# Performance work log

Hardware: AMD Instinct MI355X
Metric: run time of the kernel (lower is better)

The kernel has to match this reference:

```python
import jax, jax.numpy as jnp
import numpy as np

N = 100000   # nodes
E = 1600000  # edges
IN = 128     # in_node_channels
H = 128      # hidden_channels
EPS = 1e-5   # BatchNorm eps


def _gcn_conv(x, W, b, src, dst, n):
    # x' = W x, then symmetric-normalized aggregation with self-loops (PyG GCNConv)
    xw = x @ W                                             # [N, H]
    loop = jnp.arange(n, dtype=src.dtype)
    src_f = jnp.concatenate([src, loop])                   # [E+N]
    dst_f = jnp.concatenate([dst, loop])
    deg = jax.ops.segment_sum(jnp.ones(src_f.shape, xw.dtype), dst_f, num_segments=n)
    dis = jax.lax.rsqrt(jnp.maximum(deg, 1.0))             # deg >= 1 due to self-loops
    norm = dis[src_f] * dis[dst_f]                         # [E+N]
    msg = xw[src_f] * norm[:, None]                        # gather + scale
    out = jax.ops.segment_sum(msg, dst_f, num_segments=n)  # scatter-add
    return out + b


def _bn(x, gamma, beta):
    # training-mode BatchNorm1d over the node dimension
    m = jnp.mean(x, axis=0)
    v = jnp.mean(jnp.square(x - m), axis=0)
    return gamma * (x - m) * jax.lax.rsqrt(v + EPS) + beta


def setup_inputs() -> dict:
    key = jax.random.key(0)
    ks = jax.random.split(key, 8)
    glorot = lambda k, shape, fan: jax.random.normal(k, shape, jnp.float32) / np.sqrt(fan).astype(np.float32)
    x = jax.random.normal(ks[0], (N, IN), jnp.float32)
    edge_index = jax.random.randint(ks[1], (2, E), 0, N, dtype=jnp.int32)
    return {
        "x": x,
        "edge_index": edge_index,
        "W1": glorot(ks[2], (IN, H), IN), "b1": jnp.zeros((H,), jnp.float32),
        "g1": jnp.ones((H,), jnp.float32), "be1": jnp.zeros((H,), jnp.float32),
        "W2": glorot(ks[3], (H, H), H), "b2": jnp.zeros((H,), jnp.float32),
        "g2": jnp.ones((H,), jnp.float32), "be2": jnp.zeros((H,), jnp.float32),
        "Wm1": glorot(ks[4], (H, 64), H), "bm1": jnp.zeros((64,), jnp.float32),
        "Wm2": glorot(ks[5], (64, 1), 64), "bm2": jnp.zeros((1,), jnp.float32),
    }


def reference(x, edge_index, W1, b1, g1, be1, W2, b2, g2, be2, Wm1, bm1, Wm2, bm2):
    src, dst = edge_index[0], edge_index[1]
    h = jax.nn.relu(_bn(_gcn_conv(x, W1, b1, src, dst, N), g1, be1))
    h = jax.nn.relu(_bn(_gcn_conv(h, W2, b2, src, dst, N), g2, be2))
    # MLP head (dropout is identity in eval / deterministic reference)
    h = jax.nn.relu(h @ Wm1 + bm1)
    out = h @ Wm2 + bm2                                     # [N, 1]
    return jnp.squeeze(out, axis=-1)                        # [N]
```

## Files before the change

### kernel.cpp

```cpp
#include <hip/hip_runtime.h>
#include <hip/hip_fp16.h>

#define HC 128
#define EPS_BN 1e-5f
#define NSTRIPE 8
#define AGG_BLOCKS 3072
#define BSHIFT 9
#define BNODES (1 << BSHIFT)
#define BCAP 12288
#define CHUNK 8192
#define SRC_BITS 18

typedef _Float16 f16;
typedef f16  f16x8 __attribute__((ext_vector_type(8)));
typedef float f32x4 __attribute__((ext_vector_type(4)));

__global__ __launch_bounds__(1024) void edge_bin(const int* __restrict__ src,
                                                 const int* __restrict__ dst,
                                                 int* __restrict__ gcur,
                                                 unsigned int* __restrict__ packed, int E) {
    __shared__ int cnt[256];
    __shared__ int cur[256];
    const int tid = threadIdx.x;
    const int e0 = blockIdx.x * CHUNK;
    int dreg[8];
    if (tid < 256) cnt[tid] = 0;
    __syncthreads();
#pragma unroll
    for (int i = 0; i < 8; ++i) {
        int e = e0 + i * 1024 + tid;
        dreg[i] = (e < E) ? dst[e] : -1;
        if (dreg[i] >= 0) atomicAdd(&cnt[dreg[i] >> BSHIFT], 1);
    }
    __syncthreads();
    if (tid < 256) cur[tid] = (cnt[tid] > 0) ? atomicAdd(&gcur[tid], cnt[tid]) : 0;
    __syncthreads();
#pragma unroll
    for (int i = 0; i < 8; ++i) {
        int e = e0 + i * 1024 + tid;
        if (dreg[i] >= 0) {
            int s = src[e];
            int b = dreg[i] >> BSHIFT;
            int pos = b * BCAP + atomicAdd(&cur[b], 1);
            packed[pos] = ((unsigned)(dreg[i] & (BNODES - 1)) << SRC_BITS) | (unsigned)s;
        }
    }
}

__global__ __launch_bounds__(1024) void sort_wprep(const unsigned int* __restrict__ packed,
                                                   const int* __restrict__ gcur,
                                                   int2* __restrict__ rowptr2,
                                                   float* __restrict__ dis,
                                                   int* __restrict__ srcs, int n, int nbSort,
                                                   const float* __restrict__ W1,
                                                   const float* __restrict__ W2,
                                                   const float* __restrict__ Wm1,
                                                   f16* __restrict__ Wt1,
                                                   f16* __restrict__ Wt2,
                                                   f16* __restrict__ Wm1t) {
    if (blockIdx.x >= nbSort) {
        int idx = (blockIdx.x - nbSort) * 1024 + threadIdx.x;
        if (idx < 16384) {
            int k = idx >> 7, c = idx & 127;
            Wt1[(size_t)c * HC + k] = (f16)W1[idx];
        } else if (idx < 32768) {
            int i = idx - 16384;
            int k = i >> 7, c = i & 127;
            Wt2[(size_t)c * HC + k] = (f16)W2[i];
        } else if (idx < 40960) {
            int i = idx - 32768;
            int c = i >> 7, k = i & 127;
            Wm1t[(size_t)c * HC + k] = (f16)Wm1[(size_t)k * 64 + c];
        }
        return;
    }
    __shared__ int cnt[BNODES];
    __shared__ int cur[BNODES];
    __shared__ int scn[BNODES];
    const int b = blockIdx.x;
    const int node0 = b << BSHIFT;
    const int tid = threadIdx.x;
    const int base = b * BCAP;
    const int end  = base + gcur[b];

    if (tid < BNODES) cnt[tid] = 0;
    __syncthreads();
    for (int e = base + tid; e < end; e += 1024)
        atomicAdd(&cnt[packed[e] >> SRC_BITS], 1);
    __syncthreads();
    if (tid < BNODES) scn[tid] = cnt[tid];
    __syncthreads();
    for (int off = 1; off < BNODES; off <<= 1) {
        int t = 0;
        if (tid < BNODES && tid >= off) t = scn[tid - off];
        __syncthreads();
        if (tid < BNODES) scn[tid] += t;
        __syncthreads();
    }
    if (tid < BNODES) {
        int excl = scn[tid] - cnt[tid];
        int node = node0 + tid;
        if (node < n) {
            rowptr2[node] = make_int2(base + excl, base + excl + cnt[tid]);
            dis[node] = rsqrtf((float)cnt[tid] + 1.f);
        }
        cur[tid] = excl;
    }
    __syncthreads();
    for (int e = base + tid; e < end; e += 1024) {
        unsigned p = packed[e];
        int pos = atomicAdd(&cur[p >> SRC_BITS], 1);
        srcs[base + pos] = (int)(p & ((1u << SRC_BITS) - 1));
    }
}

template<int SRC_F16, int TRANS>
__global__ __launch_bounds__(512) void gemm_mfma(const void* __restrict__ Xv,
                                                 const f16* __restrict__ Wt,
                                                 const float* __restrict__ stats,
                                                 const float* __restrict__ gamma,
                                                 const float* __restrict__ beta,
                                                 const float* __restrict__ dis,
                                                 f16* __restrict__ Y, int n) {
    __shared__ f16 Ah[128][136];
    __shared__ f16 Bh[128][136];
    __shared__ float sc[HC], sh[HC];
    const int tid  = threadIdx.x;
    const int row0 = blockIdx.x * 128;

    if constexpr (TRANS) {
        if (tid < 128) {
            float s = 0.f, q = 0.f;
#pragma unroll
            for (int t = 0; t < NSTRIPE; ++t) {
                s += stats[t * 256 + tid];
                q += stats[t * 256 + 128 + tid];
            }
            float m = s / (float)n;
            float v = q / (float)n - m * m;
            float scv = gamma[tid] * rsqrtf(fmaxf(v, 0.f) + EPS_BN);
            sc[tid] = scv;
            sh[tid] = beta[tid] - m * scv;
        }
    }

#pragma unroll
    for (int i = 0; i < 4; ++i) {
        int idx = i * 512 + tid;
        int r = idx >> 4, g = idx & 15;
        *(f16x8*)&Bh[r][g * 8] = *(const f16x8*)(Wt + (size_t)r * HC + g * 8);
    }
    __syncthreads();

#pragma unroll
    for (int i = 0; i < 4; ++i) {
        int idx = i * 512 + tid;
        int r = idx >> 4, g = idx & 15;
        int grow = row0 + r;
        f16x8 h = {};
        if (grow < n) {
            if constexpr (SRC_F16) {
                f16x8 v = *(const f16x8*)((const f16*)Xv + (size_t)grow * HC + g * 8);
                if constexpr (TRANS) {
#pragma unroll
                    for (int j = 0; j < 8; ++j) {
                        float f = (float)v[j];
                        f = fmaxf(fmaf(f, sc[g * 8 + j], sh[g * 8 + j]), 0.f);
                        h[j] = (f16)f;
                    }
                } else h = v;
            } else {
                const float* X = (const float*)Xv;
                float4 a = *(const float4*)(X + (size_t)grow * HC + g * 8);
                float4 c = *(const float4*)(X + (size_t)grow * HC + g * 8 + 4);
                h[0] = (f16)a.x; h[1] = (f16)a.y; h[2] = (f16)a.z; h[3] = (f16)a.w;
                h[4] = (f16)c.x; h[5] = (f16)c.y; h[6] = (f16)c.z; h[7] = (f16)c.w;
            }
        }
        *(f16x8*)&Ah[r][g * 8] = h;
    }
    __syncthreads();

    const int wv   = tid >> 6;
    const int lane = tid & 63;
    const int m    = lane & 15;
    const int kq   = (lane >> 4) * 8;

    f32x4 acc[8] = {};
#pragma unroll
    for (int kc = 0; kc < HC; kc += 32) {
        f16x8 a = *(const f16x8*)&Ah[wv * 16 + m][kc + kq];
#pragma unroll
        for (int t = 0; t < 8; ++t) {
            f16x8 b = *(const f16x8*)&Bh[t * 16 + m][kc + kq];
            acc[t] = __builtin_amdgcn_mfma_f32_16x16x32_f16(a, b, acc[t], 0, 0, 0);
        }
    }

    __syncthreads();
    {
        const int rg = (lane >> 4) * 4;
        float dv[4];
#pragma unroll
        for (int r = 0; r < 4; ++r) {
            int grow = row0 + wv * 16 + rg + r;
            dv[r] = (grow < n) ? dis[grow] : 0.f;
        }
#pragma unroll
        for (int t = 0; t < 8; ++t)
#pragma unroll
            for (int r = 0; r < 4; ++r)
                Ah[wv * 16 + rg + r][t * 16 + m] = (f16)(acc[t][r] * dv[r]);
    }
    __syncthreads();
#pragma unroll
    for (int i = 0; i < 4; ++i) {
        int idx = i * 512 + tid;
        int r = idx >> 4, g = idx & 15;
        int grow = row0 + r;
        if (grow < n)
            *(f16x8*)(Y + (size_t)grow * HC + g * 8) = *(const f16x8*)&Ah[r][g * 8];
    }
}

__global__ __launch_bounds__(256) void gcn_agg_f16(const f16* __restrict__ xws,
                                                   const int* __restrict__ srcs,
                                                   const int2* __restrict__ rowptr2,
                                                   const float* __restrict__ dis,
                                                   const float* __restrict__ bias,
                                                   f16* __restrict__ out,
                                                   float* __restrict__ stats,
                                                   int n, int nwaves) {
    __shared__ float lds_s[4][128], lds_q[4][128];
    const int wv   = threadIdx.x >> 6;
    const int lane = threadIdx.x & 63;
    const int g    = lane >> 4;
    const int cg   = lane & 15;

    float b8[8];
#pragma unroll
    for (int j = 0; j < 8; ++j) b8[j] = bias[cg * 8 + j];

    float s8[8] = {}, q8[8] = {};

    for (int node = blockIdx.x * 4 + wv; node < n; node += nwaves) {
        const int2 rp = rowptr2[node];
        const int e1 = rp.y;
        float acc[8] = {};
        int e  = rp.x;
        int i0 = e + g, i1 = i0 + 4;
        int s0 = (i0 < e1) ? srcs[i0] : n;
        int s1 = (i1 < e1) ? srcs[i1] : n;
        while (e < e1) {
            int en = e + 8;
            int j0 = en + g, j1 = j0 + 4;
            int t0 = (j0 < e1) ? srcs[j0] : n;
            int t1 = (j1 < e1) ? srcs[j1] : n;
            f16x8 v0 = *(const f16x8*)(xws + (size_t)s0 * HC + cg * 8);
            f16x8 v1 = *(const f16x8*)(xws + (size_t)s1 * HC + cg * 8);
            f16x8 p = v0 + v1;
#pragma unroll
            for (int j = 0; j < 8; ++j)
                acc[j] += (float)p[j];
            s0 = t0; s1 = t1; e = en;
        }
#pragma unroll
        for (int j = 0; j < 8; ++j) acc[j] += __shfl_xor(acc[j], 16);
#pragma unroll
        for (int j = 0; j < 8; ++j) acc[j] += __shfl_xor(acc[j], 32);

        if (g == 0) {
            float dv = dis[node];
            f16x8 self = *(const f16x8*)(xws + (size_t)node * HC + cg * 8);
            f16x8 o;
#pragma unroll
            for (int j = 0; j < 8; ++j) {
                float r = fmaf(acc[j] + (float)self[j], dv, b8[j]);
                o[j] = (f16)r;
                s8[j] += r;
                q8[j] += r * r;
            }
            *(f16x8*)(out + (size_t)node * HC + cg * 8) = o;
        }
    }

    if (g == 0) {
#pragma unroll
        for (int j = 0; j < 8; ++j) {
            lds_s[wv][cg * 8 + j] = s8[j];
            lds_q[wv][cg * 8 + j] = q8[j];
        }
    }
    __syncthreads();
    float* stripe = stats + (size_t)(blockIdx.x & (NSTRIPE - 1)) * 256;
    if (threadIdx.x < 128) {
        float s = lds_s[0][threadIdx.x] + lds_s[1][threadIdx.x] +
                  lds_s[2][threadIdx.x] + lds_s[3][threadIdx.x];
        float q = lds_q[0][threadIdx.x] + lds_q[1][threadIdx.x] +
                  lds_q[2][threadIdx.x] + lds_q[3][threadIdx.x];
        atomicAdd(&stripe[threadIdx.x], s);
        atomicAdd(&stripe[128 + threadIdx.x], q);
    }
}

__global__ __launch_bounds__(256) void mlp_mfma(const f16* __restrict__ h,
                                                const float* __restrict__ stats,
                                                const float* __restrict__ gamma,
                                                const float* __restrict__ beta,
                                                const f16* __restrict__ Wm1t,
                                                const float* __restrict__ bm1,
                                                const float* __restrict__ Wm2,
                                                const float* __restrict__ bm2,
                                                float* __restrict__ out, int n) {
    __shared__ f16 Hs[64][136];
    __shared__ f16 Ws[64][136];
    __shared__ float sc[HC], sh[HC], bmv[64], w2v[64];
    const int tid  = threadIdx.x;
    const int row0 = blockIdx.x * 64;

    if (tid < 128) {
        float s = 0.f, q = 0.f;
#pragma unroll
        for (int t = 0; t < NSTRIPE; ++t) {
            s += stats[t * 256 + tid];
            q += stats[t * 256 + 128 + tid];
        }
        float m = s / (float)n;
        float v = q / (float)n - m * m;
        float scv = gamma[tid] * rsqrtf(fmaxf(v, 0.f) + EPS_BN);
        sc[tid] = scv;
        sh[tid] = beta[tid] - m * scv;
    }
    if (tid < 64) { bmv[tid] = bm1[tid]; w2v[tid] = Wm2[tid]; }

#pragma unroll
    for (int i = 0; i < 4; ++i) {
        int idx = i * 256 + tid;
        int r = idx >> 4, g = idx & 15;
        *(f16x8*)&Ws[r][g * 8] = *(const f16x8*)(Wm1t + (size_t)r * HC + g * 8);
    }
    __syncthreads();

#pragma unroll
    for (int i = 0; i < 4; ++i) {
        int idx = i * 256 + tid;
        int r = idx >> 4, g = idx & 15;
        int grow = row0 + r;
        f16x8 hv = {};
        if (grow < n) {
            f16x8 v = *(const f16x8*)(h + (size_t)grow * HC + g * 8);
#pragma unroll
            for (int j = 0; j < 8; ++j) {
                float f = (float)v[j];
                f = fmaxf(fmaf(f, sc[g * 8 + j], sh[g * 8 + j]), 0.f);
                hv[j] = (f16)f;
            }
        }
        *(f16x8*)&Hs[r][g * 8] = hv;
    }
    __syncthreads();

    const int wv   = tid >> 6;
    const int lane = tid & 63;
    const int m    = lane & 15;
    const int kq   = (lane >> 4) * 8;

    f32x4 acc[4] = {};
#pragma unroll
    for (int kc = 0; kc < HC; kc += 32) {
        f16x8 a = *(const f16x8*)&Hs[wv * 16 + m][kc + kq];
#pragma unroll
        for (int t = 0; t < 4; ++t) {
            f16x8 b = *(const f16x8*)&Ws[t * 16 + m][kc + kq];
            acc[t] = __builtin_amdgcn_mfma_f32_16x16x32_f16(a, b, acc[t], 0, 0, 0);
        }
    }

    float part[4];
#pragma unroll
    for (int reg = 0; reg < 4; ++reg) {
        float s = 0.f;
#pragma unroll
        for (int t = 0; t < 4; ++t) {
            int col = t * 16 + m;
            s += fmaxf(acc[t][reg] + bmv[col], 0.f) * w2v[col];
        }
        part[reg] = s;
    }
#pragma unroll
    for (int off = 1; off < 16; off <<= 1) {
#pragma unroll
        for (int reg = 0; reg < 4; ++reg)
            part[reg] += __shfl_xor(part[reg], off);
    }
    if (m == 0) {
        int rbase = row0 + wv * 16 + (lane >> 4) * 4;
        float bb = bm2[0];
#pragma unroll
        for (int reg = 0; reg < 4; ++reg) {
            int row = rbase + reg;
            if (row < n) out[row] = part[reg] + bb;
        }
    }
}

extern "C" void kernel_launch(void* const* d_in, const int* in_sizes, int n_in,
                              void* d_out, int out_size, void* d_ws, size_t ws_size,
                              hipStream_t stream) {
    const float* x   = (const float*)d_in[0];
    const int*   ei  = (const int*)  d_in[1];
    const float* W1  = (const float*)d_in[2];
    const float* b1  = (const float*)d_in[3];
    const float* g1  = (const float*)d_in[4];
    const float* be1 = (const float*)d_in[5];
    const float* W2  = (const float*)d_in[6];
    const float* b2  = (const float*)d_in[7];
    const float* g2  = (const float*)d_in[8];
    const float* be2 = (const float*)d_in[9];
    const float* Wm1 = (const float*)d_in[10];
    const float* bm1 = (const float*)d_in[11];
    const float* Wm2 = (const float*)d_in[12];
    const float* bm2 = (const float*)d_in[13];
    float* out = (float*)d_out;

    const int n = in_sizes[0] / HC;
    const int E = in_sizes[1] / 2;
    const int* srcp = ei;
    const int* dstp = ei + E;
    const int nb = (n + BNODES - 1) >> BSHIFT;

    char* ws = (char*)d_ws;
    size_t off = 0;
    auto alloc = [&](size_t bytes) { void* p = ws + off; off = (off + bytes + 511) & ~511ULL; return p; };
    float*  dis     = (float*) alloc((size_t)n * 4);
    int2*   rowptr2 = (int2*)  alloc((size_t)n * 8);
    int*    gcur    = (int*)   alloc(1024);
    float*  stats   = (float*) alloc(2 * NSTRIPE * 256 * 4);
    float*  stats1  = stats;
    float*  stats2  = stats + NSTRIPE * 256;
    unsigned int* packed = (unsigned int*)alloc((size_t)nb * BCAP * 4);
    int*    srcs    = (int*)   alloc((size_t)nb * BCAP * 4);
    f16*    xws     = (f16*)   alloc((size_t)(n + 1) * HC * 2);
    f16*    bufBh   = (f16*)   alloc((size_t)n * HC * 2);
    f16*    Wt1     = (f16*)   alloc((size_t)HC * HC * 2);
    f16*    Wt2     = (f16*)   alloc((size_t)HC * HC * 2);
    f16*    Wm1t    = (f16*)   alloc((size_t)64 * HC * 2);

    const int gemmBlocks = (n + 127) / 128;
    const int mlpBlocks  = (n + 63) / 64;
    const int binBlocks  = (E + CHUNK - 1) / CHUNK;
    const int wprepBlks  = 40;
    const int aggWaves   = AGG_BLOCKS * 4;

    hipMemsetAsync(gcur, 0, 1024 + 2 * NSTRIPE * 256 * 4, stream);
    hipMemsetAsync(xws + (size_t)n * HC, 0, HC * 2, stream);

    edge_bin<<<binBlocks, 1024, 0, stream>>>(srcp, dstp, gcur, packed, E);
    sort_wprep<<<nb + wprepBlks, 1024, 0, stream>>>(packed, gcur, rowptr2, dis, srcs, n, nb,
                                                    W1, W2, Wm1, Wt1, Wt2, Wm1t);

    gemm_mfma<0, 0><<<gemmBlocks, 512, 0, stream>>>(x, Wt1, nullptr, nullptr, nullptr,
                                                    dis, xws, n);
    gcn_agg_f16<<<AGG_BLOCKS, 256, 0, stream>>>(xws, srcs, rowptr2, dis, b1,
                                                bufBh, stats1, n, aggWaves);

    gemm_mfma<1, 1><<<gemmBlocks, 512, 0, stream>>>(bufBh, Wt2, stats1, g1, be1,
                                                    dis, xws, n);
    gcn_agg_f16<<<AGG_BLOCKS, 256, 0, stream>>>(xws, srcs, rowptr2, dis, b2,
                                                bufBh, stats2, n, aggWaves);

    mlp_mfma<<<mlpBlocks, 256, 0, stream>>>(bufBh, stats2, g2, be2, Wm1t, bm1, Wm2, bm2,
                                            out, n);
}
```

Baseline: 313.9 us.

## Fuse edge binning with first GEMM and move degree scaling into sort

The edge-binning pass, the first-layer GEMM (now reading fp32 W1 directly and transposing it into shared memory) and the weight prep for W2/Wm1 are merged into one launch, so the GEMM no longer waits on degree computation. The dis scaling of xw is applied afterwards in the sort kernel, which rescales each bin's rows in place. The aggregation loop is also widened to four gathers per iteration for more memory-level parallelism. The costs are an extra read-modify-write of xws in the sort kernel and a strided fp32 W1 load repeated in every GEMM block.

Result: slower. 329.1 us (+4.9%).

```diff
diff --git a/kernel.cpp b/kernel.cpp
--- a/kernel.cpp
+++ b/kernel.cpp
@@ -15,118 +15,19 @@
 typedef f16  f16x8 __attribute__((ext_vector_type(8)));
 typedef float f32x4 __attribute__((ext_vector_type(4)));
 
-__global__ __launch_bounds__(1024) void edge_bin(const int* __restrict__ src,
-                                                 const int* __restrict__ dst,
-                                                 int* __restrict__ gcur,
-                                                 unsigned int* __restrict__ packed, int E) {
-    __shared__ int cnt[256];
-    __shared__ int cur[256];
+struct GemmSmem {
+    f16 Ah[128][136];
+    f16 Bh[128][136];
+    float sc[HC], sh[HC];
+};
+
+template<int SRC_F16, int TRANS, int SCALE, int SELFW>
+__device__ __forceinline__ void gemm_body(GemmSmem& sm, int row0,
+        const void* __restrict__ Xv, const f16* __restrict__ Wt,
+        const float* __restrict__ W32, const float* __restrict__ stats,
+        const float* __restrict__ gamma, const float* __restrict__ beta,
+        const float* __restrict__ dis, f16* __restrict__ Y, int n) {
     const int tid = threadIdx.x;
-    const int e0 = blockIdx.x * CHUNK;
-    int dreg[8];
-    if (tid < 256) cnt[tid] = 0;
-    __syncthreads();
-#pragma unroll
-    for (int i = 0; i < 8; ++i) {
-        int e = e0 + i * 1024 + tid;
-        dreg[i] = (e < E) ? dst[e] : -1;
-        if (dreg[i] >= 0) atomicAdd(&cnt[dreg[i] >> BSHIFT], 1);
-    }
-    __syncthreads();
-    if (tid < 256) cur[tid] = (cnt[tid] > 0) ? atomicAdd(&gcur[tid], cnt[tid]) : 0;
-    __syncthreads();
-#pragma unroll
-    for (int i = 0; i < 8; ++i) {
-        int e = e0 + i * 1024 + tid;
-        if (dreg[i] >= 0) {
-            int s = src[e];
-            int b = dreg[i] >> BSHIFT;
-            int pos = b * BCAP + atomicAdd(&cur[b], 1);
-            packed[pos] = ((unsigned)(dreg[i] & (BNODES - 1)) << SRC_BITS) | (unsigned)s;
-        }
-    }
-}
-
-__global__ __launch_bounds__(1024) void sort_wprep(const unsigned int* __restrict__ packed,
-                                                   const int* __restrict__ gcur,
-                                                   int2* __restrict__ rowptr2,
-                                                   float* __restrict__ dis,
-                                                   int* __restrict__ srcs, int n, int nbSort,
-                                                   const float* __restrict__ W1,
-                                                   const float* __restrict__ W2,
-                                                   const float* __restrict__ Wm1,
-                                                   f16* __restrict__ Wt1,
-                                                   f16* __restrict__ Wt2,
-                                                   f16* __restrict__ Wm1t) {
-    if (blockIdx.x >= nbSort) {
-        int idx = (blockIdx.x - nbSort) * 1024 + threadIdx.x;
-        if (idx < 16384) {
-            int k = idx >> 7, c = idx & 127;
-            Wt1[(size_t)c * HC + k] = (f16)W1[idx];
-        } else if (idx < 32768) {
-            int i = idx - 16384;
-            int k = i >> 7, c = i & 127;
-            Wt2[(size_t)c * HC + k] = (f16)W2[i];
-        } else if (idx < 40960) {
-            int i = idx - 32768;
-            int c = i >> 7, k = i & 127;
-            Wm1t[(size_t)c * HC + k] = (f16)Wm1[(size_t)k * 64 + c];
-        }
-        return;
-    }
-    __shared__ int cnt[BNODES];
-    __shared__ int cur[BNODES];
-    __shared__ int scn[BNODES];
-    const int b = blockIdx.x;
-    const int node0 = b << BSHIFT;
-    const int tid = threadIdx.x;
-    const int base = b * BCAP;
-    const int end  = base + gcur[b];
-
-    if (tid < BNODES) cnt[tid] = 0;
-    __syncthreads();
-    for (int e = base + tid; e < end; e += 1024)
-        atomicAdd(&cnt[packed[e] >> SRC_BITS], 1);
-    __syncthreads();
-    if (tid < BNODES) scn[tid] = cnt[tid];
-    __syncthreads();
-    for (int off = 1; off < BNODES; off <<= 1) {
-        int t = 0;
-        if (tid < BNODES && tid >= off) t = scn[tid - off];
-        __syncthreads();
-        if (tid < BNODES) scn[tid] += t;
-        __syncthreads();
-    }
-    if (tid < BNODES) {
-        int excl = scn[tid] - cnt[tid];
-        int node = node0 + tid;
-        if (node < n) {
-            rowptr2[node] = make_int2(base + excl, base + excl + cnt[tid]);
-            dis[node] = rsqrtf((float)cnt[tid] + 1.f);
-        }
-        cur[tid] = excl;
-    }
-    __syncthreads();
-    for (int e = base + tid; e < end; e += 1024) {
-        unsigned p = packed[e];
-        int pos = atomicAdd(&cur[p >> SRC_BITS], 1);
-        srcs[base + pos] = (int)(p & ((1u << SRC_BITS) - 1));
-    }
-}
-
-template<int SRC_F16, int TRANS>
-__global__ __launch_bounds__(512) void gemm_mfma(const void* __restrict__ Xv,
-                                                 const f16* __restrict__ Wt,
-                                                 const float* __restrict__ stats,
-                                                 const float* __restrict__ gamma,
-                                                 const float* __restrict__ beta,
-                                                 const float* __restrict__ dis,
-                                                 f16* __restrict__ Y, int n) {
-    __shared__ f16 Ah[128][136];
-    __shared__ f16 Bh[128][136];
-    __shared__ float sc[HC], sh[HC];
-    const int tid  = threadIdx.x;
-    const int row0 = blockIdx.x * 128;
 
     if constexpr (TRANS) {
         if (tid < 128) {
@@ -139,16 +40,27 @@
             float m = s / (float)n;
             float v = q / (float)n - m * m;
             float scv = gamma[tid] * rsqrtf(fmaxf(v, 0.f) + EPS_BN);
-            sc[tid] = scv;
-            sh[tid] = beta[tid] - m * scv;
-        }
-    }
-
-#pragma unroll
-    for (int i = 0; i < 4; ++i) {
-        int idx = i * 512 + tid;
-        int r = idx >> 4, g = idx & 15;
-        *(f16x8*)&Bh[r][g * 8] = *(const f16x8*)(Wt + (size_t)r * HC + g * 8);
+            sm.sc[tid] = scv;
+            sm.sh[tid] = beta[tid] - m * scv;
+        }
+    }
+
+    if constexpr (SELFW) {
+#pragma unroll
+        for (int i = 0; i < 4; ++i) {
+            int idx = i * 512 + tid;
+            int g = idx >> 7, r = idx & 127;
+#pragma unroll
+            for (int j = 0; j < 8; ++j)
+                sm.Bh[r][g * 8 + j] = (f16)W32[(size_t)(g * 8 + j) * HC + r];
+        }
+    } else {
+#pragma unroll
+        for (int i = 0; i < 4; ++i) {
+            int idx = i * 512 + tid;
+            int r = idx >> 4, g = idx & 15;
+            *(f16x8*)&sm.Bh[r][g * 8] = *(const f16x8*)(Wt + (size_t)r * HC + g * 8);
+        }
     }
     __syncthreads();
 
@@ -165,7 +77,7 @@
 #pragma unroll
                     for (int j = 0; j < 8; ++j) {
                         float f = (float)v[j];
-                        f = fmaxf(fmaf(f, sc[g * 8 + j], sh[g * 8 + j]), 0.f);
+                        f = fmaxf(fmaf(f, sm.sc[g * 8 + j], sm.sh[g * 8 + j]), 0.f);
                         h[j] = (f16)f;
                     }
                 } else h = v;
@@ -177,7 +89,7 @@
                 h[4] = (f16)c.x; h[5] = (f16)c.y; h[6] = (f16)c.z; h[7] = (f16)c.w;
             }
         }
-        *(f16x8*)&Ah[r][g * 8] = h;
+        *(f16x8*)&sm.Ah[r][g * 8] = h;
     }
     __syncthreads();
 
@@ -189,10 +101,10 @@
     f32x4 acc[8] = {};
 #pragma unroll
     for (int kc = 0; kc < HC; kc += 32) {
-        f16x8 a = *(const f16x8*)&Ah[wv * 16 + m][kc + kq];
+        f16x8 a = *(const f16x8*)&sm.Ah[wv * 16 + m][kc + kq];
 #pragma unroll
         for (int t = 0; t < 8; ++t) {
-            f16x8 b = *(const f16x8*)&Bh[t * 16 + m][kc + kq];
+            f16x8 b = *(const f16x8*)&sm.Bh[t * 16 + m][kc + kq];
             acc[t] = __builtin_amdgcn_mfma_f32_16x16x32_f16(a, b, acc[t], 0, 0, 0);
         }
     }
@@ -203,14 +115,16 @@
         float dv[4];
 #pragma unroll
         for (int r = 0; r < 4; ++r) {
-            int grow = row0 + wv * 16 + rg + r;
-            dv[r] = (grow < n) ? dis[grow] : 0.f;
+            if constexpr (SCALE) {
+                int grow = row0 + wv * 16 + rg + r;
+                dv[r] = (grow < n) ? dis[grow] : 0.f;
+            } else dv[r] = 1.f;
         }
 #pragma unroll
         for (int t = 0; t < 8; ++t)
 #pragma unroll
             for (int r = 0; r < 4; ++r)
-                Ah[wv * 16 + rg + r][t * 16 + m] = (f16)(acc[t][r] * dv[r]);
+                sm.Ah[wv * 16 + rg + r][t * 16 + m] = (f16)(acc[t][r] * dv[r]);
     }
     __syncthreads();
 #pragma unroll
@@ -219,8 +133,136 @@
         int r = idx >> 4, g = idx & 15;
         int grow = row0 + r;
         if (grow < n)
-            *(f16x8*)(Y + (size_t)grow * HC + g * 8) = *(const f16x8*)&Ah[r][g * 8];
-    }
+            *(f16x8*)(Y + (size_t)grow * HC + g * 8) = *(const f16x8*)&sm.Ah[r][g * 8];
+    }
+}
+
+__global__ __launch_bounds__(512) void fused_bin_gemm(
+        const int* __restrict__ src, const int* __restrict__ dst,
+        int* __restrict__ gcur, unsigned int* __restrict__ packed, int E,
+        const float* __restrict__ x, const float* __restrict__ W1,
+        f16* __restrict__ xws, int n, int binBlocks, int gemmBlocks,
+        const float* __restrict__ W2, const float* __restrict__ Wm1,
+        f16* __restrict__ Wt2, f16* __restrict__ Wm1t) {
+    __shared__ GemmSmem sm;
+    const int bi = blockIdx.x;
+    if (bi < binBlocks) {
+        int* cnt = (int*)&sm;
+        int* cur = cnt + 256;
+        const int tid = threadIdx.x;
+        if (bi == 0 && tid < HC) xws[(size_t)n * HC + tid] = (f16)0.f;
+        const int e0 = bi * CHUNK;
+        int dreg[16];
+        if (tid < 256) cnt[tid] = 0;
+        __syncthreads();
+#pragma unroll
+        for (int i = 0; i < 16; ++i) {
+            int e = e0 + i * 512 + tid;
+            dreg[i] = (e < E) ? dst[e] : -1;
+            if (dreg[i] >= 0) atomicAdd(&cnt[dreg[i] >> BSHIFT], 1);
+        }
+        __syncthreads();
+        if (tid < 256) cur[tid] = (cnt[tid] > 0) ? atomicAdd(&gcur[tid], cnt[tid]) : 0;
+        __syncthreads();
+#pragma unroll
+        for (int i = 0; i < 16; ++i) {
+            int e = e0 + i * 512 + tid;
+            if (dreg[i] >= 0) {
+                int s = src[e];
+                int b = dreg[i] >> BSHIFT;
+                int pos = b * BCAP + atomicAdd(&cur[b], 1);
+                packed[pos] = ((unsigned)(dreg[i] & (BNODES - 1)) << SRC_BITS) | (unsigned)s;
+            }
+        }
+    } else if (bi < binBlocks + gemmBlocks) {
+        gemm_body<0, 0, 0, 1>(sm, (bi - binBlocks) * 128, x, nullptr, W1,
+                              nullptr, nullptr, nullptr, nullptr, xws, n);
+    } else {
+        int idx = (bi - binBlocks - gemmBlocks) * 512 + threadIdx.x;
+        if (idx < 16384) {
+            int k = idx >> 7, c = idx & 127;
+            Wt2[(size_t)c * HC + k] = (f16)W2[idx];
+        } else if (idx < 24576) {
+            int i = idx - 16384;
+            int c = i >> 7, k = i & 127;
+            Wm1t[(size_t)c * HC + k] = (f16)Wm1[(size_t)k * 64 + c];
+        }
+    }
+}
+
+__global__ __launch_bounds__(1024) void sort_scale(const unsigned int* __restrict__ packed,
+                                                   const int* __restrict__ gcur,
+                                                   int2* __restrict__ rowptr2,
+                                                   float* __restrict__ dis,
+                                                   int* __restrict__ srcs,
+                                                   f16* __restrict__ xws, int n) {
+    __shared__ int cnt[BNODES];
+    __shared__ int cur[BNODES];
+    __shared__ int scn[BNODES];
+    __shared__ float dsc[BNODES];
+    const int b = blockIdx.x;
+    const int node0 = b << BSHIFT;
+    const int tid = threadIdx.x;
+    const int base = b * BCAP;
+    const int end  = base + gcur[b];
+
+    if (tid < BNODES) cnt[tid] = 0;
+    __syncthreads();
+    for (int e = base + tid; e < end; e += 1024)
+        atomicAdd(&cnt[packed[e] >> SRC_BITS], 1);
+    __syncthreads();
+    if (tid < BNODES) {
+        float dv = rsqrtf((float)cnt[tid] + 1.f);
+        dsc[tid] = dv;
+        int node = node0 + tid;
+        if (node < n) dis[node] = dv;
+        scn[tid] = cnt[tid];
+    }
+    __syncthreads();
+    for (int idx = tid; idx < BNODES * 16; idx += 1024) {
+        int r = idx >> 4, gg = idx & 15;
+        int node = node0 + r;
+        if (node < n) {
+            f16x8* p = (f16x8*)(xws + (size_t)node * HC + gg * 8);
+            f16x8 v = *p;
+            float dv = dsc[r];
+#pragma unroll
+            for (int j = 0; j < 8; ++j) v[j] = (f16)((float)v[j] * dv);
+            *p = v;
+        }
+    }
+    for (int off = 1; off < BNODES; off <<= 1) {
+        int t = 0;
+        if (tid < BNODES && tid >= off) t = scn[tid - off];
+        __syncthreads();
+        if (tid < BNODES) scn[tid] += t;
+        __syncthreads();
+    }
+    if (tid < BNODES) {
+        int excl = scn[tid] - cnt[tid];
+        int node = node0 + tid;
+        if (node < n)
+            rowptr2[node] = make_int2(base + excl, base + excl + cnt[tid]);
+        cur[tid] = excl;
+    }
+    __syncthreads();
+    for (int e = base + tid; e < end; e += 1024) {
+        unsigned p = packed[e];
+        int pos = atomicAdd(&cur[p >> SRC_BITS], 1);
+        srcs[base + pos] = (int)(p & ((1u << SRC_BITS) - 1));
+    }
+}
+
+__global__ __launch_bounds__(512) void gemm_k(const void* __restrict__ Xv,
+                                              const f16* __restrict__ Wt,
+                                              const float* __restrict__ stats,
+                                              const float* __restrict__ gamma,
+                                              const float* __restrict__ beta,
+                                              const float* __restrict__ dis,
+                                              f16* __restrict__ Y, int n) {
+    __shared__ GemmSmem sm;
+    gemm_body<1, 1, 1, 0>(sm, blockIdx.x * 128, Xv, Wt, nullptr,
+                          stats, gamma, beta, dis, Y, n);
 }
 
 __global__ __launch_bounds__(256) void gcn_agg_f16(const f16* __restrict__ xws,
@@ -248,21 +290,28 @@
         const int e1 = rp.y;
         float acc[8] = {};
         int e  = rp.x;
-        int i0 = e + g, i1 = i0 + 4;
+        int i0 = e + g, i1 = i0 + 4, i2 = i0 + 8, i3 = i0 + 12;
         int s0 = (i0 < e1) ? srcs[i0] : n;
         int s1 = (i1 < e1) ? srcs[i1] : n;
+        int s2 = (i2 < e1) ? srcs[i2] : n;
+        int s3 = (i3 < e1) ? srcs[i3] : n;
         while (e < e1) {
-            int en = e + 8;
-            int j0 = en + g, j1 = j0 + 4;
+            int en = e + 16;
+            int j0 = en + g, j1 = j0 + 4, j2 = j0 + 8, j3 = j0 + 12;
             int t0 = (j0 < e1) ? srcs[j0] : n;
             int t1 = (j1 < e1) ? srcs[j1] : n;
+            int t2 = (j2 < e1) ? srcs[j2] : n;
+            int t3 = (j3 < e1) ? srcs[j3] : n;
             f16x8 v0 = *(const f16x8*)(xws + (size_t)s0 * HC + cg * 8);
             f16x8 v1 = *(const f16x8*)(xws + (size_t)s1 * HC + cg * 8);
-            f16x8 p = v0 + v1;
+            f16x8 v2 = *(const f16x8*)(xws + (size_t)s2 * HC + cg * 8);
+            f16x8 v3 = *(const f16x8*)(xws + (size_t)s3 * HC + cg * 8);
+            f16x8 p01 = v0 + v1;
+            f16x8 p23 = v2 + v3;
 #pragma unroll
             for (int j = 0; j < 8; ++j)
-                acc[j] += (float)p[j];
-            s0 = t0; s1 = t1; e = en;
+                acc[j] += (float)p01[j] + (float)p23[j];
+            s0 = t0; s1 = t1; s2 = t2; s3 = t3; e = en;
         }
 #pragma unroll
         for (int j = 0; j < 8; ++j) acc[j] += __shfl_xor(acc[j], 16);
@@ -442,30 +491,28 @@
     int*    srcs    = (int*)   alloc((size_t)nb * BCAP * 4);
     f16*    xws     = (f16*)   alloc((size_t)(n + 1) * HC * 2);
     f16*    bufBh   = (f16*)   alloc((size_t)n * HC * 2);
-    f16*    Wt1     = (f16*)   alloc((size_t)HC * HC * 2);
     f16*    Wt2     = (f16*)   alloc((size_t)HC * HC * 2);
     f16*    Wm1t    = (f16*)   alloc((size_t)64 * HC * 2);
 
     const int gemmBlocks = (n + 127) / 128;
     const int mlpBlocks  = (n + 63) / 64;
     const int binBlocks  = (E + CHUNK - 1) / CHUNK;
-    const int wprepBlks  = 40;
+    const int wprepBlks  = 48;
     const int aggWaves   = AGG_BLOCKS * 4;
 
     hipMemsetAsync(gcur, 0, 1024 + 2 * NSTRIPE * 256 * 4, stream);
-    hipMemsetAsync(xws + (size_t)n * HC, 0, HC * 2, stream);
-
-    edge_bin<<<binBlocks, 1024, 0, stream>>>(srcp, dstp, gcur, packed, E);
-    sort_wprep<<<nb + wprepBlks, 1024, 0, stream>>>(packed, gcur, rowptr2, dis, srcs, n, nb,
-                                                    W1, W2, Wm1, Wt1, Wt2, Wm1t);
-
-    gemm_mfma<0, 0><<<gemmBlocks, 512, 0, stream>>>(x, Wt1, nullptr, nullptr, nullptr,
-                                                    dis, xws, n);
+
+    fused_bin_gemm<<<binBlocks + gemmBlocks + wprepBlks, 512, 0, stream>>>(
+        srcp, dstp, gcur, packed, E, x, W1, xws, n, binBlocks, gemmBlocks,
+        W2, Wm1, Wt2, Wm1t);
+
+    sort_scale<<<nb, 1024, 0, stream>>>(packed, gcur, rowptr2, dis, srcs, xws, n);
+
     gcn_agg_f16<<<AGG_BLOCKS, 256, 0, stream>>>(xws, srcs, rowptr2, dis, b1,
                                                 bufBh, stats1, n, aggWaves);
 
-    gemm_mfma<1, 1><<<gemmBlocks, 512, 0, stream>>>(bufBh, Wt2, stats1, g1, be1,
-                                                    dis, xws, n);
+    gemm_k<<<gemmBlocks, 512, 0, stream>>>(bufBh, Wt2, stats1, g1, be1,
+                                           dis, xws, n);
     gcn_agg_f16<<<AGG_BLOCKS, 256, 0, stream>>>(xws, srcs, rowptr2, dis, b2,
                                                 bufBh, stats2, n, aggWaves);
 
```
